# Kernel optimization log

Hardware: AMD Instinct MI355X
Metric: run time of the kernel (lower is better)

The kernel has to match this reference:

```python
import jax, jax.numpy as jnp
import numpy as np

DIM, HEADS, DIM_HEAD = 1024, 16, 64
INNER = HEADS * DIM_HEAD  # 1024
FF = 4 * DIM
EPS = 1e-5


def layer_norm(x, g, b):
    mu = jnp.mean(x, axis=-1, keepdims=True)
    var = jnp.mean(jnp.square(x - mu), axis=-1, keepdims=True)
    return (x - mu) * jax.lax.rsqrt(var + EPS) * g + b


def setup_inputs() -> dict:
    key = jax.random.key(0)
    ks = jax.random.split(key, 8)
    B, N = 2, 2048
    s = 0.02
    return {
        "x": jax.random.normal(ks[0], (B, N, DIM), dtype=jnp.float32),
        "ln1_g": jnp.ones((DIM,), jnp.float32),
        "ln1_b": jnp.zeros((DIM,), jnp.float32),
        "ln2_g": jnp.ones((DIM,), jnp.float32),
        "ln2_b": jnp.zeros((DIM,), jnp.float32),
        "w_qkv": jax.random.normal(ks[1], (DIM, 3 * INNER), jnp.float32) * s,
        "w_out": jax.random.normal(ks[2], (INNER, DIM), jnp.float32) * s,
        "b_out": jnp.zeros((DIM,), jnp.float32),
        "w_ff1": jax.random.normal(ks[3], (DIM, FF), jnp.float32) * s,
        "b_ff1": jnp.zeros((FF,), jnp.float32),
        "w_ff2": jax.random.normal(ks[4], (FF, DIM), jnp.float32) * s,
        "b_ff2": jnp.zeros((DIM,), jnp.float32),
    }


def reference(x, ln1_g, ln1_b, ln2_g, ln2_b, w_qkv, w_out, b_out,
              w_ff1, b_ff1, w_ff2, b_ff2):
    B, N, _ = x.shape
    scale = DIM_HEAD ** -0.5
    h = layer_norm(x, ln1_g, ln1_b)
    qkv = h @ w_qkv  # [B, N, 3*INNER]
    q, k, v = jnp.split(qkv, 3, axis=-1)
    # b n (h d) -> b h n d
    def to_heads(t):
        return t.reshape(B, N, HEADS, DIM_HEAD).transpose(0, 2, 1, 3)
    q, k, v = to_heads(q), to_heads(k), to_heads(v)
    dots = jnp.einsum('bhnd,bhmd->bhnm', q, k) * scale
    attn = jax.nn.softmax(dots, axis=-1)  # dropout = identity (eval)
    out = jnp.einsum('bhnm,bhmd->bhnd', attn, v)
    out = out.transpose(0, 2, 1, 3).reshape(B, N, INNER)
    out = out @ w_out + b_out
    x = x + out  # residual
    h2 = layer_norm(x, ln2_g, ln2_b)
    ff = jax.nn.gelu(h2 @ w_ff1 + b_ff1, approximate=False) @ w_ff2 + b_ff2
    return x + ff
```

## Files before the change

### kernel.cpp

```cpp
#include <hip/hip_runtime.h>
#include <hip/hip_bf16.h>
#include <math.h>

#define SEQ   2048
#define BATCH 2
#define NROWS 4096
#define DIMM  1024
#define QKV3  3072
#define FFD   4096
#define NHEAD 16
#define DHEAD 64

typedef __bf16 bf16;
typedef __bf16 bf16x4 __attribute__((ext_vector_type(4)));
typedef __bf16 bf16x8 __attribute__((ext_vector_type(8)));
typedef float  f32x4  __attribute__((ext_vector_type(4)));

static __device__ __forceinline__ f32x4 mfma16(bf16x8 a, bf16x8 b, f32x4 c) {
    return __builtin_amdgcn_mfma_f32_16x16x32_bf16(a, b, c, 0, 0, 0);
}

#define GLDS16(gp, lp) __builtin_amdgcn_global_load_lds( \
    (__attribute__((address_space(1))) void*)(gp),       \
    (__attribute__((address_space(3))) void*)(lp), 16, 0, 0)

#define MEMFENCE asm volatile("" ::: "memory")

__global__ __launch_bounds__(256) void tcast_kernel(
    const float* __restrict__ src, bf16* __restrict__ dst, int K, int N)
{
    __shared__ float tile[32][33];
    const int n0 = blockIdx.x * 32;
    const int k0 = blockIdx.y * 32;
    const int r = threadIdx.x >> 5;
    const int c = threadIdx.x & 31;
    #pragma unroll
    for (int i = 0; i < 4; ++i)
        tile[r + 8 * i][c] = src[(size_t)(k0 + r + 8 * i) * N + n0 + c];
    __syncthreads();
    #pragma unroll
    for (int i = 0; i < 4; ++i)
        dst[(size_t)(n0 + r + 8 * i) * K + k0 + c] = (bf16)tile[c][r + 8 * i];
}

__global__ __launch_bounds__(256) void ln_cast_kernel(
    const float* __restrict__ x, const float* __restrict__ g,
    const float* __restrict__ b, bf16* __restrict__ out)
{
    const int row = blockIdx.x;
    const int t = threadIdx.x;
    const float4 v = ((const float4*)(x + (size_t)row * DIMM))[t];
    float s  = v.x + v.y + v.z + v.w;
    float sq = v.x * v.x + v.y * v.y + v.z * v.z + v.w * v.w;
    #pragma unroll
    for (int m = 1; m < 64; m <<= 1) {
        s  += __shfl_xor(s, m, 64);
        sq += __shfl_xor(sq, m, 64);
    }
    __shared__ float ss[4], ssq[4];
    const int wave = t >> 6;
    if ((t & 63) == 0) { ss[wave] = s; ssq[wave] = sq; }
    __syncthreads();
    s  = ss[0] + ss[1] + ss[2] + ss[3];
    sq = ssq[0] + ssq[1] + ssq[2] + ssq[3];
    const float mean = s * (1.0f / DIMM);
    const float var  = sq * (1.0f / DIMM) - mean * mean;
    const float rs   = rsqrtf(var + 1e-5f);
    const float4 gv = ((const float4*)g)[t];
    const float4 bv = ((const float4*)b)[t];
    bf16* o = out + (size_t)row * DIMM + t * 4;
    o[0] = (bf16)((v.x - mean) * rs * gv.x + bv.x);
    o[1] = (bf16)((v.y - mean) * rs * gv.y + bv.y);
    o[2] = (bf16)((v.z - mean) * rs * gv.z + bv.z);
    o[3] = (bf16)((v.w - mean) * rs * gv.w + bv.w);
}

template<int EPI>
__global__ __launch_bounds__(512, 2)
void gemm256_kernel(const bf16* __restrict__ A, const bf16* __restrict__ BT,
                    const float* __restrict__ bias, bf16* __restrict__ C,
                    int M, int N, int K, int ld)
{
    __shared__ bf16 As_[2][2][8192];
    __shared__ bf16 Bs_[2][2][8192];
    const int nb = N >> 8;
    const int chunk = (int)gridDim.x >> 3;
    const int idx = ((int)blockIdx.x & 7) * chunk + ((int)blockIdx.x >> 3);
    const int bm = idx / nb, bn = idx - bm * nb;
    const int tm = bm << 8, tn = bn << 8;
    const int tid = threadIdx.x;
    const int lane = tid & 63, w = tid >> 6;
    const int wr = w >> 2, wc = w & 3;
    const int lq = lane & 15, hk = lane >> 4;

    const int sr  = lane >> 3;
    const int sgo = (((lane & 7) ^ sr) << 3);
    const bf16* gA0 = A  + (size_t)(tm +       w * 8 + sr) * ld + sgo;
    const bf16* gA1 = A  + (size_t)(tm + 128 + w * 8 + sr) * ld + sgo;
    const bf16* gB0 = BT + (size_t)(tn +       w * 8 + sr) * ld + sgo;
    const bf16* gB1 = BT + (size_t)(tn + 128 + w * 8 + sr) * ld + sgo;
    const size_t l64 = (size_t)64 * ld;

#define STG_A0(D, T) do { const size_t ko_ = (size_t)(T) * 64;              \
        GLDS16(gA0 + ko_,       &As_[D][0][w * 512]);                       \
        GLDS16(gA0 + ko_ + l64, &As_[D][0][4096 + w * 512]); } while (0)
#define STG_A1(D, T) do { const size_t ko_ = (size_t)(T) * 64;              \
        GLDS16(gA1 + ko_,       &As_[D][1][w * 512]);                       \
        GLDS16(gA1 + ko_ + l64, &As_[D][1][4096 + w * 512]); } while (0)
#define STG_B0(D, T) do { const size_t ko_ = (size_t)(T) * 64;              \
        GLDS16(gB0 + ko_,       &Bs_[D][0][w * 512]);                       \
        GLDS16(gB0 + ko_ + l64, &Bs_[D][0][4096 + w * 512]); } while (0)
#define STG_B1(D, T) do { const size_t ko_ = (size_t)(T) * 64;              \
        GLDS16(gB1 + ko_,       &Bs_[D][1][w * 512]);                       \
        GLDS16(gB1 + ko_ + l64, &Bs_[D][1][4096 + w * 512]); } while (0)

    f32x4 acc[8][4] = {};
    const int NT = K >> 6;

    STG_A0(0, 0); STG_B1(0, 0); STG_B0(0, 0); STG_A1(0, 0);
    STG_B0(1, 1); STG_A1(1, 1);

    for (int t = 0; t < NT; ++t) {
        const int d = t & 1, e = d ^ 1;
        if (t == NT - 1) asm volatile("s_waitcnt vmcnt(0)" ::: "memory");
        else             asm volatile("s_waitcnt vmcnt(4)" ::: "memory");
        __builtin_amdgcn_s_barrier();
        MEMFENCE;

        const char* Ah0 = (const char*)&As_[d][0][0];
        const char* Ah1 = (const char*)&As_[d][1][0];
        const char* Bh0 = (const char*)&Bs_[d][0][0];
        const char* Bh1 = (const char*)&Bs_[d][1][0];
        bf16x8 af[4][2], bfv[2][2];

#define DO_MFMA(MH, NH) do {                                                 \
        __builtin_amdgcn_s_setprio(1);                                       \
        _Pragma("unroll")                                                    \
        for (int mi = 0; mi < 4; ++mi)                                       \
            _Pragma("unroll")                                                \
            for (int nj = 0; nj < 2; ++nj)                                   \
                _Pragma("unroll")                                            \
                for (int kk = 0; kk < 2; ++kk)                               \
                    acc[(MH)*4+mi][(NH)*2+nj] =                              \
                        mfma16(bfv[nj][kk], af[mi][kk], acc[(MH)*4+mi][(NH)*2+nj]); \
        __builtin_amdgcn_s_setprio(0); } while (0)

        {
            #pragma unroll
            for (int mi = 0; mi < 4; ++mi) {
                const int lr = wr * 64 + mi * 16 + lq;
                af[mi][0] = *(const bf16x8*)(Ah0 + lr * 128 + ((hk ^ (lr & 7)) << 4));
                af[mi][1] = *(const bf16x8*)(Ah0 + lr * 128 + (((4 + hk) ^ (lr & 7)) << 4));
            }
            #pragma unroll
            for (int nj = 0; nj < 2; ++nj) {
                const int lc = wc * 32 + nj * 16 + lq;
                bfv[nj][0] = *(const bf16x8*)(Bh0 + lc * 128 + ((hk ^ (lc & 7)) << 4));
                bfv[nj][1] = *(const bf16x8*)(Bh0 + lc * 128 + (((4 + hk) ^ (lc & 7)) << 4));
            }
            if (t + 1 < NT) STG_A0(e, t + 1);
            DO_MFMA(0, 0);
        }
        MEMFENCE; __builtin_amdgcn_s_barrier(); MEMFENCE;
        {
            #pragma unroll
            for (int mi = 0; mi < 4; ++mi) {
                const int lr = wr * 64 + mi * 16 + lq;
                af[mi][0] = *(const bf16x8*)(Ah1 + lr * 128 + ((hk ^ (lr & 7)) << 4));
                af[mi][1] = *(const bf16x8*)(Ah1 + lr * 128 + (((4 + hk) ^ (lr & 7)) << 4));
            }
            if (t + 1 < NT) STG_B1(e, t + 1);
            DO_MFMA(1, 0);
        }
        MEMFENCE; __builtin_amdgcn_s_barrier(); MEMFENCE;
        {
            #pragma unroll
            for (int nj = 0; nj < 2; ++nj) {
                const int lc = wc * 32 + nj * 16 + lq;
                bfv[nj][0] = *(const bf16x8*)(Bh1 + lc * 128 + ((hk ^ (lc & 7)) << 4));
                bfv[nj][1] = *(const bf16x8*)(Bh1 + lc * 128 + (((4 + hk) ^ (lc & 7)) << 4));
            }
            if (t + 2 < NT) STG_B0(d, t + 2);
            DO_MFMA(1, 1);
        }
        MEMFENCE; __builtin_amdgcn_s_barrier(); MEMFENCE;
        {
            #pragma unroll
            for (int mi = 0; mi < 4; ++mi) {
                const int lr = wr * 64 + mi * 16 + lq;
                af[mi][0] = *(const bf16x8*)(Ah0 + lr * 128 + ((hk ^ (lr & 7)) << 4));
                af[mi][1] = *(const bf16x8*)(Ah0 + lr * 128 + (((4 + hk) ^ (lr & 7)) << 4));
            }
            if (t + 2 < NT) STG_A1(d, t + 2);
            DO_MFMA(0, 1);
        }
        MEMFENCE; __builtin_amdgcn_s_barrier(); MEMFENCE;
#undef DO_MFMA
    }
#undef STG_A0
#undef STG_A1
#undef STG_B0
#undef STG_B1

    #pragma unroll
    for (int i = 0; i < 8; ++i) {
        const int mh = i >> 2, mi = i & 3;
        const int row = tm + mh * 128 + wr * 64 + mi * 16 + lq;
        #pragma unroll
        for (int j = 0; j < 4; ++j) {
            const int nh = j >> 1, nj = j & 1;
            const int col = tn + nh * 128 + wc * 32 + nj * 16 + (hk << 2);
            if (EPI == 0) {
                bf16x4 pk = { (bf16)acc[i][j][0], (bf16)acc[i][j][1],
                              (bf16)acc[i][j][2], (bf16)acc[i][j][3] };
                *(bf16x4*)(C + (size_t)row * N + col) = pk;
            } else {
                const float4 bv4 = *(const float4*)(bias + col);
                float v0 = acc[i][j][0] + bv4.x, v1 = acc[i][j][1] + bv4.y;
                float v2 = acc[i][j][2] + bv4.z, v3 = acc[i][j][3] + bv4.w;
                bf16x4 pk = {
                    (bf16)(0.5f * v0 * (1.0f + erff(v0 * 0.70710678118654752f))),
                    (bf16)(0.5f * v1 * (1.0f + erff(v1 * 0.70710678118654752f))),
                    (bf16)(0.5f * v2 * (1.0f + erff(v2 * 0.70710678118654752f))),
                    (bf16)(0.5f * v3 * (1.0f + erff(v3 * 0.70710678118654752f))) };
                *(bf16x4*)(C + (size_t)row * N + col) = pk;
            }
        }
    }
}

template<int EPI>
__global__ __launch_bounds__(256, 3)
void gemm_bt_kernel(const bf16* __restrict__ A, const bf16* __restrict__ BT,
                    const float* __restrict__ bias, const float* __restrict__ res,
                    void* __restrict__ Cout, int M, int N, int K, int ld)
{
    __shared__ bf16 As[3][4096];
    __shared__ bf16 Bs[3][4096];
    const int nb = N >> 7;
    const int chunk = (int)gridDim.x >> 3;
    int idx = (blockIdx.x & 7) * chunk + (blockIdx.x >> 3);
    int ks = 0;
    if (EPI == 3) {
        const int tiles = (M >> 7) * nb;
        ks = idx / tiles;
        idx -= ks * tiles;
    }
    const int bm = idx / nb, bn = idx - bm * nb;
    const int tm = bm << 7, tn = bn << 7;
    const int tid = threadIdx.x;
    const int lane = tid & 63, wave = tid >> 6;
    const int wm = (wave >> 1) << 6, wn = (wave & 1) << 6;
    const int kofs = ks * K;

    const bf16* ga = A  + (size_t)(tm + wave * 32 + (lane >> 2)) * ld + kofs + ((lane & 3) << 3);
    const bf16* gb = BT + (size_t)(tn + wave * 32 + (lane >> 2)) * ld + kofs + ((lane & 3) << 3);
    const size_t k16 = (size_t)16 * ld;

    f32x4 acc[4][4] = {};
    const int ro = (lane & 15) * 32 + ((lane >> 4) << 3);

#define GSTAGE(BUF, KO) do {                          \
        bf16* la_ = &As[BUF][wave * 1024];            \
        bf16* lb_ = &Bs[BUF][wave * 1024];            \
        GLDS16(ga + (KO),       la_);                 \
        GLDS16(ga + (KO) + k16, la_ + 512);           \
        GLDS16(gb + (KO),       lb_);                 \
        GLDS16(gb + (KO) + k16, lb_ + 512);           \
    } while (0)

    GSTAGE(0, 0);
    GSTAGE(1, 32);
    GSTAGE(2, 64);
    int cur = 0;
    for (int k0 = 0; k0 < K; k0 += 32) {
        if (k0 + 96 <= K)      asm volatile("s_waitcnt vmcnt(8)" ::: "memory");
        else if (k0 + 64 <= K) asm volatile("s_waitcnt vmcnt(4)" ::: "memory");
        else                   asm volatile("s_waitcnt vmcnt(0)" ::: "memory");
        __builtin_amdgcn_s_barrier();

        bf16x8 af[4], bfr[4];
        #pragma unroll
        for (int i = 0; i < 4; ++i) {
            af[i]  = *(const bf16x8*)(&As[cur][0] + (wm + i * 16) * 32 + ro);
            bfr[i] = *(const bf16x8*)(&Bs[cur][0] + (wn + i * 16) * 32 + ro);
        }
        #pragma unroll
        for (int i = 0; i < 4; ++i)
            #pragma unroll
            for (int j = 0; j < 4; ++j)
                acc[i][j] = mfma16(bfr[j], af[i], acc[i][j]);

        MEMFENCE;
        __builtin_amdgcn_s_barrier();
        MEMFENCE;
        if (k0 + 96 < K) GSTAGE(cur, k0 + 96);
        cur = (cur == 2) ? 0 : cur + 1;
    }
#undef GSTAGE

    const int lq = lane & 15, hk = lane >> 4;
    const int r0 = tm + wm + lq;
    const int c0 = tn + wn + (hk << 2);
    if (EPI == 1) {
        float* C = (float*)Cout;
        #pragma unroll
        for (int j = 0; j < 4; ++j) {
            const float4 bv4 = *(const float4*)(bias + c0 + j * 16);
            #pragma unroll
            for (int i = 0; i < 4; ++i) {
                const size_t off = (size_t)(r0 + i * 16) * N + c0 + j * 16;
                const float4 rv = *(const float4*)(res + off);
                float4 o;
                o.x = acc[i][j][0] + bv4.x + rv.x;
                o.y = acc[i][j][1] + bv4.y + rv.y;
                o.z = acc[i][j][2] + bv4.z + rv.z;
                o.w = acc[i][j][3] + bv4.w + rv.w;
                *(float4*)(C + off) = o;
            }
        }
    } else {
        float* C = (float*)(ks == 0 ? Cout : (void*)res);
        #pragma unroll
        for (int j = 0; j < 4; ++j)
            #pragma unroll
            for (int i = 0; i < 4; ++i) {
                float4 o = { acc[i][j][0], acc[i][j][1], acc[i][j][2], acc[i][j][3] };
                *(float4*)(C + (size_t)(r0 + i * 16) * N + c0 + j * 16) = o;
            }
    }
}

__global__ __launch_bounds__(256) void ff2_reduce_kernel(
    const float* __restrict__ p0, const float* __restrict__ p1,
    const float* __restrict__ bias, const float* __restrict__ res,
    float* __restrict__ out)
{
    const int i = blockIdx.x * 256 + threadIdx.x;
    const float4 a = ((const float4*)p0)[i];
    const float4 b = ((const float4*)p1)[i];
    const float4 r = ((const float4*)res)[i];
    const float4 g = ((const float4*)bias)[i & 255];
    float4 o;
    o.x = a.x + b.x + r.x + g.x;
    o.y = a.y + b.y + r.y + g.y;
    o.z = a.z + b.z + r.z + g.z;
    o.w = a.w + b.w + r.w + g.w;
    ((float4*)out)[i] = o;
}

__global__ __launch_bounds__(256) void vtrans_kernel(
    const bf16* __restrict__ qkv, bf16* __restrict__ vT)
{
    __shared__ bf16 t[64 * 64];
    const int n0 = blockIdx.x * 64;
    const int bh = blockIdx.y;
    const int b = bh >> 4, h = bh & 15;
    const bf16* src = qkv + (size_t)(b * SEQ + n0) * QKV3 + 2 * DIMM + h * DHEAD;

    #pragma unroll
    for (int it = 0; it < 2; ++it) {
        const int c = it * 256 + threadIdx.x;
        const int n = c >> 3, d8 = (c & 7) * 8;
        const bf16x8 v8 = *(const bf16x8*)(src + (size_t)n * QKV3 + d8);
        const int byte = (n * 128 + d8 * 2) ^ (((n >> 3) & 7) << 4);
        *(bf16x8*)((char*)t + byte) = v8;
    }
    __syncthreads();
    #pragma unroll
    for (int it = 0; it < 2; ++it) {
        const int c = it * 256 + threadIdx.x;
        const int d = c >> 3, nc = c & 7;
        bf16x8 o8;
        #pragma unroll
        for (int i = 0; i < 8; ++i) {
            const int n = nc * 8 + i;
            const int byte = (n * 128 + d * 2) ^ ((nc & 7) << 4);
            o8[i] = *(const bf16*)((const char*)t + byte);
        }
        *(bf16x8*)(vT + (size_t)bh * DHEAD * SEQ + (size_t)d * SEQ + n0 + nc * 8) = o8;
    }
}

__global__ __launch_bounds__(256, 4)
void attn_kernel(const bf16* __restrict__ qkv, const bf16* __restrict__ vT,
                 bf16* __restrict__ out)
{
    __shared__ bf16 Ks[2][64 * 64];
    __shared__ bf16 Vs[2][64 * 64];
    __shared__ bf16 Ps[4][16 * 64];
    const int bid = blockIdx.x;
    const int idx = (bid & 7) * 128 + (bid >> 3);
    const int qt = idx & 31;
    const int bh = idx >> 5;
    const int b = bh >> 4, h = bh & 15;
    const int tid = threadIdx.x;
    const int lane = tid & 63, wave = tid >> 6;
    const int q = lane & 15, hi = lane >> 4;

    const bf16* qbase = qkv + (size_t)(b * SEQ) * QKV3 + h * DHEAD;
    const bf16* kbase = qbase + DIMM;
    const bf16* vbase = vT + (size_t)bh * DHEAD * SEQ;

    const int q0 = qt * 64 + wave * 16;
    bf16x8 qf[2];
    {
        const bf16* qp = qbase + (size_t)(q0 + q) * QKV3 + (hi << 3);
        qf[0] = *(const bf16x8*)qp;
        qf[1] = *(const bf16x8*)(qp + 32);
        #pragma unroll
        for (int j = 0; j < 8; ++j) {
            qf[0][j] = (bf16)((float)qf[0][j] * 0.125f);
            qf[1][j] = (bf16)((float)qf[1][j] * 0.125f);
        }
    }

    const int srow = lane >> 3;
    const int scol = ((lane & 7) ^ srow) << 3;
    const bf16* gk = kbase + (size_t)(wave * 16 + srow) * QKV3 + scol;
    const bf16* gv = vbase + (size_t)(wave * 16 + srow) * SEQ + scol;

#define STAGE(BUF, KT) do {                                        \
        bf16* lk_ = &Ks[BUF][wave * 1024];                         \
        bf16* lv_ = &Vs[BUF][wave * 1024];                         \
        GLDS16(gk + (size_t)(KT) * QKV3,       lk_);               \
        GLDS16(gk + (size_t)((KT) + 8) * QKV3, lk_ + 512);         \
        GLDS16(gv + (KT),                      lv_);               \
        GLDS16(gv + (KT) + 8 * SEQ,            lv_ + 512);         \
    } while (0)

    float m = -1e30f, l = 0.0f;
    f32x4 o[4] = {};

    STAGE(0, 0);
    int cur = 0;
    for (int kt = 0; kt < SEQ; kt += 64) {
        __syncthreads();
        if (kt + 64 < SEQ) STAGE(cur ^ 1, kt + 64);

        f32x4 sv[4];
        __builtin_amdgcn_s_setprio(1);
        #pragma unroll
        for (int kf = 0; kf < 4; ++kf) {
            f32x4 z = {0.f, 0.f, 0.f, 0.f};
            sv[kf] = z;
            #pragma unroll
            for (int ks = 0; ks < 2; ++ks) {
                const int row = kf * 16 + q;
                const int bo = (row * 128 + ks * 64 + (hi << 4)) ^ ((row & 7) << 4);
                const bf16x8 kfrag = *(const bf16x8*)((const char*)&Ks[cur][0] + bo);
                sv[kf] = mfma16(kfrag, qf[ks], sv[kf]);
            }
        }
        __builtin_amdgcn_s_setprio(0);

        float pmax;
        {
            float a = fmaxf(fmaxf(sv[0][0], sv[0][1]), fmaxf(sv[0][2], sv[0][3]));
            float b2 = fmaxf(fmaxf(sv[1][0], sv[1][1]), fmaxf(sv[1][2], sv[1][3]));
            float c = fmaxf(fmaxf(sv[2][0], sv[2][1]), fmaxf(sv[2][2], sv[2][3]));
            float d = fmaxf(fmaxf(sv[3][0], sv[3][1]), fmaxf(sv[3][2], sv[3][3]));
            pmax = fmaxf(fmaxf(a, b2), fmaxf(c, d));
        }
        pmax = fmaxf(pmax, __shfl_xor(pmax, 16, 64));
        pmax = fmaxf(pmax, __shfl_xor(pmax, 32, 64));

        if (__any(pmax - m > 8.0f)) {
            const float nm = fmaxf(m, pmax);
            const float fr = __expf(m - nm);
            l *= fr;
            #pragma unroll
            for (int df = 0; df < 4; ++df) {
                o[df][0] *= fr; o[df][1] *= fr;
                o[df][2] *= fr; o[df][3] *= fr;
            }
            m = nm;
        }

        float rsum = 0.0f;
        #pragma unroll
        for (int kf = 0; kf < 4; ++kf) {
            float p0 = __expf(sv[kf][0] - m);
            float p1 = __expf(sv[kf][1] - m);
            float p2 = __expf(sv[kf][2] - m);
            float p3 = __expf(sv[kf][3] - m);
            rsum += (p0 + p1) + (p2 + p3);
            bf16x4 pk = { (bf16)p0, (bf16)p1, (bf16)p2, (bf16)p3 };
            const int bo = (q * 128 + kf * 32 + hi * 8) ^ ((q & 7) << 4);
            *(bf16x4*)((char*)Ps[wave] + bo) = pk;
        }
        rsum += __shfl_xor(rsum, 16, 64);
        rsum += __shfl_xor(rsum, 32, 64);
        l += rsum;

        bf16x8 pf[2];
        #pragma unroll
        for (int ks = 0; ks < 2; ++ks) {
            const int bo = (q * 128 + ks * 64 + (hi << 4)) ^ ((q & 7) << 4);
            pf[ks] = *(const bf16x8*)((const char*)Ps[wave] + bo);
        }
        __builtin_amdgcn_s_setprio(1);
        #pragma unroll
        for (int df = 0; df < 4; ++df)
            #pragma unroll
            for (int ks = 0; ks < 2; ++ks) {
                const int rowv = df * 16 + q;
                const int bo = (rowv * 128 + ks * 64 + (hi << 4)) ^ ((rowv & 7) << 4);
                const bf16x8 vfrag = *(const bf16x8*)((const char*)&Vs[cur][0] + bo);
                o[df] = mfma16(vfrag, pf[ks], o[df]);
            }
        __builtin_amdgcn_s_setprio(0);
        cur ^= 1;
    }
#undef STAGE

    {
        const float inv = 1.0f / l;
        const int grow = b * SEQ + q0 + q;
        #pragma unroll
        for (int df = 0; df < 4; ++df) {
            bf16x4 pk = { (bf16)(o[df][0] * inv), (bf16)(o[df][1] * inv),
                          (bf16)(o[df][2] * inv), (bf16)(o[df][3] * inv) };
            *(bf16x4*)(out + (size_t)grow * DIMM + h * DHEAD + df * 16 + hi * 4) = pk;
        }
    }
}

extern "C" void kernel_launch(void* const* d_in, const int* in_sizes, int n_in,
                              void* d_out, int out_size, void* d_ws, size_t ws_size,
                              hipStream_t stream)
{
    (void)in_sizes; (void)n_in; (void)out_size;
    const float* x    = (const float*)d_in[0];
    const float* ln1g = (const float*)d_in[1];
    const float* ln1b = (const float*)d_in[2];
    const float* ln2g = (const float*)d_in[3];
    const float* ln2b = (const float*)d_in[4];
    const float* wqkv = (const float*)d_in[5];
    const float* wout = (const float*)d_in[6];
    const float* bout = (const float*)d_in[7];
    const float* wff1 = (const float*)d_in[8];
    const float* bff1 = (const float*)d_in[9];
    const float* wff2 = (const float*)d_in[10];
    const float* bff2 = (const float*)d_in[11];

    char* ws = (char*)d_ws;
    const dim3 blk(256);
    const dim3 blk512(512);
    const bool splitk = ws_size >= 92274688ULL;

    if (splitk) {
        bf16*  wff2T = (bf16*)(ws);
        bf16*  woutT = (bf16*)(ws + 8388608);
        bf16*  wff1T = (bf16*)(ws + 10485760);
        bf16*  wqkvT = (bf16*)(ws + 18874368);
        bf16*  hbuf  = (bf16*)(ws + 25165824);
        bf16*  qkvb  = (bf16*)(ws + 33554432);
        bf16*  vT    = (bf16*)(ws + 58720256);
        bf16*  attnb = (bf16*)(ws + 67108864);
        float* x2    = (float*)(ws + 75497472);
        bf16*  fbuf  = (bf16*)(ws + 41943040);
        float* p0    = (float*)(ws + 8388608);
        float* p1    = (float*)(ws + 25165824);

        tcast_kernel<<<dim3(QKV3 / 32, DIMM / 32), blk, 0, stream>>>(wqkv, wqkvT, DIMM, QKV3);
        tcast_kernel<<<dim3(DIMM / 32, DIMM / 32), blk, 0, stream>>>(wout, woutT, DIMM, DIMM);
        tcast_kernel<<<dim3(FFD  / 32, DIMM / 32), blk, 0, stream>>>(wff1, wff1T, DIMM, FFD);
        tcast_kernel<<<dim3(DIMM / 32, FFD  / 32), blk, 0, stream>>>(wff2, wff2T, FFD, DIMM);

        ln_cast_kernel<<<NROWS, blk, 0, stream>>>(x, ln1g, ln1b, hbuf);
        gemm256_kernel<0><<<(NROWS / 256) * (QKV3 / 256), blk512, 0, stream>>>(
            hbuf, wqkvT, nullptr, qkvb, NROWS, QKV3, DIMM, DIMM);
        vtrans_kernel<<<dim3(SEQ / 64, BATCH * NHEAD), blk, 0, stream>>>(qkvb, vT);
        attn_kernel<<<dim3(1024), blk, 0, stream>>>(qkvb, vT, attnb);
        gemm_bt_kernel<1><<<(NROWS / 128) * (DIMM / 128), blk, 0, stream>>>(
            attnb, woutT, bout, x, x2, NROWS, DIMM, DIMM, DIMM);
        ln_cast_kernel<<<NROWS, blk, 0, stream>>>(x2, ln2g, ln2b, hbuf);
        gemm256_kernel<2><<<(NROWS / 256) * (FFD / 256), blk512, 0, stream>>>(
            hbuf, wff1T, bff1, fbuf, NROWS, FFD, DIMM, DIMM);
        gemm_bt_kernel<3><<<2 * (NROWS / 128) * (DIMM / 128), blk, 0, stream>>>(
            fbuf, wff2T, nullptr, (const float*)p1, p0, NROWS, DIMM, FFD / 2, FFD);
        ff2_reduce_kernel<<<(NROWS * DIMM) / 1024, blk, 0, stream>>>(
            p0, p1, bff2, x2, (float*)d_out);
    } else {
        bf16*  wqkvT = (bf16*)(ws);
        bf16*  woutT = (bf16*)(ws + 6291456);
        bf16*  wff1T = (bf16*)(ws + 8388608);
        bf16*  wff2T = (bf16*)(ws + 16777216);
        float* x2    = (float*)(ws + 25165824);
        bf16*  vT    = (bf16*)(ws + 25165824);
        bf16*  hbuf  = (bf16*)(ws + 41943040);
        bf16*  qkvb  = (bf16*)(ws + 50331648);
        bf16*  attnb = (bf16*)(ws + 75497472);
        bf16*  fbuf  = (bf16*)(ws + 50331648);

        tcast_kernel<<<dim3(QKV3 / 32, DIMM / 32), blk, 0, stream>>>(wqkv, wqkvT, DIMM, QKV3);
        tcast_kernel<<<dim3(DIMM / 32, DIMM / 32), blk, 0, stream>>>(wout, woutT, DIMM, DIMM);
        tcast_kernel<<<dim3(FFD  / 32, DIMM / 32), blk, 0, stream>>>(wff1, wff1T, DIMM, FFD);
        tcast_kernel<<<dim3(DIMM / 32, FFD  / 32), blk, 0, stream>>>(wff2, wff2T, FFD, DIMM);

        ln_cast_kernel<<<NROWS, blk, 0, stream>>>(x, ln1g, ln1b, hbuf);
        gemm256_kernel<0><<<(NROWS / 256) * (QKV3 / 256), blk512, 0, stream>>>(
            hbuf, wqkvT, nullptr, qkvb, NROWS, QKV3, DIMM, DIMM);
        vtrans_kernel<<<dim3(SEQ / 64, BATCH * NHEAD), blk, 0, stream>>>(qkvb, vT);
        attn_kernel<<<dim3(1024), blk, 0, stream>>>(qkvb, vT, attnb);
        gemm_bt_kernel<1><<<(NROWS / 128) * (DIMM / 128), blk, 0, stream>>>(
            attnb, woutT, bout, x, x2, NROWS, DIMM, DIMM, DIMM);
        ln_cast_kernel<<<NROWS, blk, 0, stream>>>(x2, ln2g, ln2b, hbuf);
        gemm256_kernel<2><<<(NROWS / 256) * (FFD / 256), blk512, 0, stream>>>(
            hbuf, wff1T, bff1, fbuf, NROWS, FFD, DIMM, DIMM);
        gemm_bt_kernel<1><<<(NROWS / 128) * (DIMM / 128), blk, 0, stream>>>(
            fbuf, wff2T, bff2, x2, (float*)d_out, NROWS, DIMM, FFD, FFD);
    }
}
```

Baseline: 268.7 us.

## Merge weight cast launches and run QKV projection on 128-tile GEMM

The four transpose-cast launches for the weights are merged into one launch that maps block indices to each weight matrix, which removes launch overhead and tail gaps between them. The QKV projection moves from the 256x256-tile GEMM to the 128x128-tile gemm_bt kernel, which gets a new bf16 output epilogue. The smaller tiles give 768 blocks instead of 192, which should fill the CUs better, at the cost of less data reuse per tile.

```diff
diff --git a/kernel.cpp b/kernel.cpp
--- a/kernel.cpp
+++ b/kernel.cpp
@@ -26,12 +26,22 @@
 
 #define MEMFENCE asm volatile("" ::: "memory")
 
-__global__ __launch_bounds__(256) void tcast_kernel(
-    const float* __restrict__ src, bf16* __restrict__ dst, int K, int N)
-{
+__global__ __launch_bounds__(256) void wcast_kernel(
+    const float* __restrict__ wqkv, bf16* __restrict__ wqkvT,
+    const float* __restrict__ wout, bf16* __restrict__ woutT,
+    const float* __restrict__ wff1, bf16* __restrict__ wff1T,
+    const float* __restrict__ wff2, bf16* __restrict__ wff2T)
+{
+    int t = blockIdx.x;
+    const float* src; bf16* dst; int K, N, nx;
+    if (t < 3072)      { src = wqkv; dst = wqkvT; K = DIMM; N = QKV3; nx = 96;  }
+    else if (t < 4096) { src = wout; dst = woutT; K = DIMM; N = DIMM; nx = 32; t -= 3072; }
+    else if (t < 8192) { src = wff1; dst = wff1T; K = DIMM; N = FFD;  nx = 128; t -= 4096; }
+    else               { src = wff2; dst = wff2T; K = FFD;  N = DIMM; nx = 32; t -= 8192; }
+    const int k0 = (t / nx) * 32;
+    const int n0 = (t - (t / nx) * nx) * 32;
+
     __shared__ float tile[32][33];
-    const int n0 = blockIdx.x * 32;
-    const int k0 = blockIdx.y * 32;
     const int r = threadIdx.x >> 5;
     const int c = threadIdx.x & 31;
     #pragma unroll
@@ -302,7 +312,17 @@
     const int lq = lane & 15, hk = lane >> 4;
     const int r0 = tm + wm + lq;
     const int c0 = tn + wn + (hk << 2);
-    if (EPI == 1) {
+    if (EPI == 0) {
+        bf16* C = (bf16*)Cout;
+        #pragma unroll
+        for (int j = 0; j < 4; ++j)
+            #pragma unroll
+            for (int i = 0; i < 4; ++i) {
+                bf16x4 pk = { (bf16)acc[i][j][0], (bf16)acc[i][j][1],
+                              (bf16)acc[i][j][2], (bf16)acc[i][j][3] };
+                *(bf16x4*)(C + (size_t)(r0 + i * 16) * N + c0 + j * 16) = pk;
+            }
+    } else if (EPI == 1) {
         float* C = (float*)Cout;
         #pragma unroll
         for (int j = 0; j < 4; ++j) {
@@ -563,14 +583,12 @@
         float* p0    = (float*)(ws + 8388608);
         float* p1    = (float*)(ws + 25165824);
 
-        tcast_kernel<<<dim3(QKV3 / 32, DIMM / 32), blk, 0, stream>>>(wqkv, wqkvT, DIMM, QKV3);
-        tcast_kernel<<<dim3(DIMM / 32, DIMM / 32), blk, 0, stream>>>(wout, woutT, DIMM, DIMM);
-        tcast_kernel<<<dim3(FFD  / 32, DIMM / 32), blk, 0, stream>>>(wff1, wff1T, DIMM, FFD);
-        tcast_kernel<<<dim3(DIMM / 32, FFD  / 32), blk, 0, stream>>>(wff2, wff2T, FFD, DIMM);
+        wcast_kernel<<<dim3(12288), blk, 0, stream>>>(
+            wqkv, wqkvT, wout, woutT, wff1, wff1T, wff2, wff2T);
 
         ln_cast_kernel<<<NROWS, blk, 0, stream>>>(x, ln1g, ln1b, hbuf);
-        gemm256_kernel<0><<<(NROWS / 256) * (QKV3 / 256), blk512, 0, stream>>>(
-            hbuf, wqkvT, nullptr, qkvb, NROWS, QKV3, DIMM, DIMM);
+        gemm_bt_kernel<0><<<(NROWS / 128) * (QKV3 / 128), blk, 0, stream>>>(
+            hbuf, wqkvT, nullptr, nullptr, qkvb, NROWS, QKV3, DIMM, DIMM);
         vtrans_kernel<<<dim3(SEQ / 64, BATCH * NHEAD), blk, 0, stream>>>(qkvb, vT);
         attn_kernel<<<dim3(1024), blk, 0, stream>>>(qkvb, vT, attnb);
         gemm_bt_kernel<1><<<(NROWS / 128) * (DIMM / 128), blk, 0, stream>>>(
@@ -594,14 +612,12 @@
         bf16*  attnb = (bf16*)(ws + 75497472);
         bf16*  fbuf  = (bf16*)(ws + 50331648);
 
-        tcast_kernel<<<dim3(QKV3 / 32, DIMM / 32), blk, 0, stream>>>(wqkv, wqkvT, DIMM, QKV3);
-        tcast_kernel<<<dim3(DIMM / 32, DIMM / 32), blk, 0, stream>>>(wout, woutT, DIMM, DIMM);
-        tcast_kernel<<<dim3(FFD  / 32, DIMM / 32), blk, 0, stream>>>(wff1, wff1T, DIMM, FFD);
-        tcast_kernel<<<dim3(DIMM / 32, FFD  / 32), blk, 0, stream>>>(wff2, wff2T, FFD, DIMM);
+        wcast_kernel<<<dim3(12288), blk, 0, stream>>>(
+            wqkv, wqkvT, wout, woutT, wff1, wff1T, wff2, wff2T);
 
         ln_cast_kernel<<<NROWS, blk, 0, stream>>>(x, ln1g, ln1b, hbuf);
-        gemm256_kernel<0><<<(NROWS / 256) * (QKV3 / 256), blk512, 0, stream>>>(
-            hbuf, wqkvT, nullptr, qkvb, NROWS, QKV3, DIMM, DIMM);
+        gemm_bt_kernel<0><<<(NROWS / 128) * (QKV3 / 128), blk, 0, stream>>>(
+            hbuf, wqkvT, nullptr, nullptr, qkvb, NROWS, QKV3, DIMM, DIMM);
         vtrans_kernel<<<dim3(SEQ / 64, BATCH * NHEAD), blk, 0, stream>>>(qkvb, vT);
         attn_kernel<<<dim3(1024), blk, 0, stream>>>(qkvb, vT, attnb);
         gemm_bt_kernel<1><<<(NROWS / 128) * (DIMM / 128), blk, 0, stream>>>(
```

Measured after the change: 263.5 us (median of 2 runs). About the same (-1.9%).
